# Performance work log

Measured on AMD Instinct MI355X. Metric: run time of the kernel, lower is better.

The kernel has to match this reference:

```python
import jax, jax.numpy as jnp
import numpy as np

EPS = 1e-7  # keras.backend.epsilon()
B, U, F = 1024, 256, 31
D = 1 + U + F  # features dim after concat


def setup_inputs() -> dict:
    key = jax.random.key(0)
    ks = jax.random.split(key, 9)
    s = 1.0 / np.sqrt(D)
    return {
        "last_cell": jax.random.uniform(ks[0], (B, U), dtype=jnp.float32),
        "input_precipitation": jax.random.uniform(ks[1], (B,), dtype=jnp.float32),
        "input_other_features": jax.random.normal(ks[2], (B, F), dtype=jnp.float32),
        "W_i": jax.random.normal(ks[3], (D, U), dtype=jnp.float32) * s,
        "b_i": jnp.zeros((U,), dtype=jnp.float32),
        "W_r": jax.random.normal(ks[4], (D, U * U), dtype=jnp.float32) * s,
        "b_r": jnp.zeros((U * U,), dtype=jnp.float32),
        "W_o": jax.random.normal(ks[5], (D, U), dtype=jnp.float32) * s,
        "b_o": jnp.zeros((U,), dtype=jnp.float32),
    }


def reference(last_cell, input_precipitation, input_other_features,
              W_i, b_i, W_r, b_r, W_o, b_o):
    # L1-normalize last cell state (mass fractions)
    l1 = jnp.sum(jnp.abs(last_cell), axis=-1, keepdims=True) + EPS
    last_cell_hat = last_cell / l1
    p = input_precipitation[:, None]  # [B,1]
    features = jnp.concatenate([p, last_cell_hat, input_other_features], axis=-1)  # [B,D]

    # input gate: sigmoid then L1-normalized across units (mass-conserving split)
    ig = jax.nn.sigmoid(features @ W_i + b_i)
    ig = ig / jnp.sum(jnp.abs(ig), axis=-1, keepdims=True)

    # redistribution matrix: relu, reshape [B,U,U], L1-normalize each row
    R = jax.nn.relu(features @ W_r + b_r).reshape(-1, U, U)
    R = R / jnp.sum(jnp.abs(R), axis=-1, keepdims=True)

    # output gate: sigmoid
    og = jax.nn.sigmoid(features @ W_o + b_o)

    cell_in = ig * p                                   # [B,U]
    cell_sys = jnp.einsum('bu,buv->bv', last_cell, R)  # batched (1xU)@(UxU)
    candidate = cell_in + cell_sys
    output = og * candidate
    cell = (1.0 - og) * candidate
    return (cell, output)
```

## Files before the change

### kernel.cpp

```cpp
#include <hip/hip_runtime.h>


#define EPS_L1 1e-7f

constexpr int BB  = 1024;
constexpr int U   = 256;
constexpr int F   = 31;
constexpr int D   = 1 + U + F;
constexpr int NBV = BB * U;
constexpr int NCH = D / 32;
constexpr int UIMGB = NCH * 16384;
constexpr size_t WTB_BYTES  = (size_t)258 * UIMGB;
constexpr size_t FEAT_BYTES = (size_t)BB * D * 2;

typedef float f32x4 __attribute__((ext_vector_type(4)));
typedef short bf16x8 __attribute__((ext_vector_type(8)));

__device__ __forceinline__ unsigned f2bf(float x) {
  union { float f; unsigned u; } v; v.f = x;
  unsigned r = v.u + 0x7FFFu + ((v.u >> 16) & 1u);
  return r >> 16;
}

__device__ __forceinline__ void barrier_lgkm() {
  asm volatile("s_waitcnt lgkmcnt(0)" ::: "memory");
  __builtin_amdgcn_sched_barrier(0);
  __builtin_amdgcn_s_barrier();
  __builtin_amdgcn_sched_barrier(0);
}

#define GLDS16(gp, lp)                                                        \
  __builtin_amdgcn_global_load_lds(                                          \
      (const __attribute__((address_space(1))) void*)(gp),                   \
      (__attribute__((address_space(3))) void*)(lp), 16, 0, 0)

#define MFMA16(a, b, c) __builtin_amdgcn_mfma_f32_16x16x32_bf16((a), (b), (c), 0, 0, 0)

__global__ __launch_bounds__(256) void k_prep(
    const float* __restrict__ lc, const float* __restrict__ p,
    const float* __restrict__ other,
    const float* __restrict__ Wi, const float* __restrict__ Wr,
    const float* __restrict__ Wo,
    short* __restrict__ WtB, short* __restrict__ featImg,
    float* __restrict__ cell_sys) {
  __shared__ unsigned tw[256][17];
  __shared__ float inv_s[64];
  const int bid = blockIdx.x, t = threadIdx.x;

  if (bid < 2322) {
    const int u = bid / 9, c = bid % 9;
    const float* src; long ld;
    if (u < 256)       { src = Wr + (size_t)u * 256; ld = 65536; }
    else if (u == 256) { src = Wi; ld = 256; }
    else               { src = Wo; ld = 256; }

    const int kp = t >> 4, f = t & 15;
    const float* r0 = src + (size_t)(c * 32 + 2 * kp) * ld;
    const float* r1 = r0 + ld;
#pragma unroll
    for (int i = 0; i < 4; ++i) {
      const int v0 = f * 4 + i * 64;
      const float4 a = *(const float4*)(r0 + v0);
      const float4 b = *(const float4*)(r1 + v0);
      tw[v0 + 0][kp] = f2bf(a.x) | (f2bf(b.x) << 16);
      tw[v0 + 1][kp] = f2bf(a.y) | (f2bf(b.y) << 16);
      tw[v0 + 2][kp] = f2bf(a.z) | (f2bf(b.z) << 16);
      tw[v0 + 3][kp] = f2bf(a.w) | (f2bf(b.w) << 16);
    }
    __syncthreads();

    const int lane = t & 63, wave = t >> 6;
    const int g = lane >> 4, l15 = lane & 15;
    short* dst = WtB + (size_t)u * 73728 + (size_t)c * 16 * 512;
#pragma unroll
    for (int ii = 0; ii < 4; ++ii) {
      const int n0 = wave * 4 + ii;
      const int row = n0 * 16 + l15;
      union { unsigned u4[4]; bf16x8 h; } cv;
#pragma unroll
      for (int j = 0; j < 4; ++j) cv.u4[j] = tw[row][g * 4 + j];
      *(bf16x8*)(dst + (size_t)n0 * 512 + lane * 8) = cv.h;
    }
  } else if (bid < 2338) {
    const int mb = bid - 2322;
    const int b0 = mb * 64;
    const int row = t >> 2, q = t & 3;
    const float4* lp = (const float4*)(lc + (size_t)(b0 + row) * 256 + q * 64);
    float s = 0.f;
#pragma unroll
    for (int j = 0; j < 16; ++j) {
      const float4 v = lp[j];
      s += fabsf(v.x) + fabsf(v.y) + fabsf(v.z) + fabsf(v.w);
    }
    s += __shfl_xor(s, 1, 64);
    s += __shfl_xor(s, 2, 64);
    if (q == 0) inv_s[row] = 1.f / (s + EPS_L1);
    __syncthreads();
#pragma unroll
    for (int i = 0; i < 9; ++i) {
      const int idx = i * 256 + t;
      const int reg = idx >> 6, l = idx & 63;
      const int c = reg >> 2, mt = reg & 3;
      const int lrow = mt * 16 + (l & 15);
      const int grow = b0 + lrow;
      const int k0 = c * 32 + (l >> 4) * 8;
      bf16x8 h;
#pragma unroll
      for (int j = 0; j < 8; ++j) {
        const int k = k0 + j;
        float v;
        if (k == 0) v = p[grow];
        else if (k <= 256) v = lc[(size_t)grow * 256 + (k - 1)] * inv_s[lrow];
        else v = other[(size_t)grow * 31 + (k - 257)];
        h[j] = (short)f2bf(v);
      }
      *(bf16x8*)(featImg + (size_t)mb * 18432 + (size_t)reg * 512 + l * 8) = h;
    }
  } else {
    float4* cs4 = (float4*)cell_sys;
    const int base = (bid - 2338) * 8192 + t;
    const float4 z = {0.f, 0.f, 0.f, 0.f};
#pragma unroll
    for (int k2 = 0; k2 < 32; ++k2) cs4[base + k2 * 256] = z;
  }
}

__global__ __launch_bounds__(512, 4) void k_heavyR10(
    const short* __restrict__ featImg, const short* __restrict__ WtB,
    const float* __restrict__ lc, const float* __restrict__ br,
    float* __restrict__ cell_sys) {
  __shared__ short aT[18432];
  __shared__ float rsum[2][64][4];
  __shared__ float lcs[8][64];

  const int t = threadIdx.x, lane = t & 63, wave = t >> 6;
  const int cq = wave & 3, rh = wave >> 2;
  const int quad = lane >> 4, l15 = lane & 15;
  const int bid = blockIdx.x;
  const int Mb = bid >> 5, ug = bid & 31;
  const int b0 = Mb * 64, u0 = ug * 8;

  {
    const char* gA = (const char*)featImg + (size_t)Mb * 36864;
    char* lA = (char*)aT;
#pragma unroll
    for (int i = 0; i < 5; ++i) {
      const int off = i * 8192 + t * 16;
      if (off < 36864) GLDS16(gA + off, lA + off);
    }
  }

  if (t < 64) {
    const float* lp = lc + (size_t)(b0 + t) * 256 + u0;
    const float4 v0 = *(const float4*)(lp);
    const float4 v1 = *(const float4*)(lp + 4);
    lcs[0][t] = v0.x; lcs[1][t] = v0.y; lcs[2][t] = v0.z; lcs[3][t] = v0.w;
    lcs[4][t] = v1.x; lcs[5][t] = v1.y; lcs[6][t] = v1.z; lcs[7][t] = v1.w;
  }

  const char* aB = (const char*)aT + rh * 2048 + lane * 16;
  const char* bB = (const char*)WtB + (size_t)u0 * UIMGB + cq * 4096 + lane * 16;

  f32x4 acc[2][4], outa[2][4];
#pragma unroll
  for (int m = 0; m < 2; ++m)
#pragma unroll
    for (int n = 0; n < 4; ++n)
#pragma unroll
      for (int r = 0; r < 4; ++r) { acc[m][n][r] = 0.f; outa[m][n][r] = 0.f; }

  bf16x8 bfr[3][4];
#pragma unroll
  for (int n = 0; n < 4; ++n) bfr[0][n] = *(const bf16x8*)(bB + n * 1024);
#pragma unroll
  for (int n = 0; n < 4; ++n) bfr[1][n] = *(const bf16x8*)(bB + 16384 + n * 1024);

  __syncthreads();

  for (int uu = 0; uu < 8; ++uu) {
    const int u = u0 + uu;
    float bv[4];

#pragma unroll
    for (int c = 0; c < 9; ++c) {
      if (c == 0) {
#pragma unroll
        for (int n = 0; n < 4; ++n)
          bv[n] = br[(size_t)u * 256 + cq * 64 + n * 16 + l15];
      }
#pragma unroll
      for (int n = 0; n < 4; ++n)
        bfr[(c + 2) % 3][n] = *(const bf16x8*)(bB + (c + 2) * 16384 + n * 1024);
      const bf16x8 a0 = *(const bf16x8*)(aB + c * 4096);
      const bf16x8 a1 = *(const bf16x8*)(aB + c * 4096 + 1024);
#pragma unroll
      for (int n = 0; n < 4; ++n) {
        acc[0][n] = MFMA16(a0, bfr[c % 3][n], acc[0][n]);
        acc[1][n] = MFMA16(a1, bfr[c % 3][n], acc[1][n]);
      }
    }
    bB += UIMGB;

    const int ub = uu & 1;
    float sm[2][4];
#pragma unroll
    for (int m = 0; m < 2; ++m)
#pragma unroll
      for (int r = 0; r < 4; ++r) {
        float sv = 0.f;
#pragma unroll
        for (int n = 0; n < 4; ++n) {
          const float rv = fmaxf(acc[m][n][r] + bv[n], 0.f);
          acc[m][n][r] = rv;
          sv += rv;
        }
        sm[m][r] = sv;
      }
#pragma unroll
    for (int msk = 1; msk < 16; msk <<= 1)
#pragma unroll
      for (int m = 0; m < 2; ++m)
#pragma unroll
        for (int r = 0; r < 4; ++r)
          sm[m][r] += __shfl_xor(sm[m][r], msk, 64);
    if (l15 == 0) {
#pragma unroll
      for (int m = 0; m < 2; ++m)
#pragma unroll
        for (int r = 0; r < 4; ++r)
          rsum[ub][rh * 32 + m * 16 + quad * 4 + r][cq] = sm[m][r];
    }
    barrier_lgkm();
#pragma unroll
    for (int m = 0; m < 2; ++m)
#pragma unroll
      for (int r = 0; r < 4; ++r) {
        const int row = rh * 32 + m * 16 + quad * 4 + r;
        const float4 rv = *(const float4*)&rsum[ub][row][0];
        const float tot = (rv.x + rv.y) + (rv.z + rv.w);
        const float alpha = lcs[uu][row] * __builtin_amdgcn_rcpf(tot);
#pragma unroll
        for (int n = 0; n < 4; ++n) {
          outa[m][n][r] = fmaf(alpha, acc[m][n][r], outa[m][n][r]);
          acc[m][n][r] = 0.f;
        }
      }
  }

#pragma unroll
  for (int m = 0; m < 2; ++m)
#pragma unroll
    for (int r = 0; r < 4; ++r) {
      const int grow = b0 + rh * 32 + m * 16 + quad * 4 + r;
#pragma unroll
      for (int n = 0; n < 4; ++n)
        atomicAdd(&cell_sys[(size_t)grow * 256 + cq * 64 + n * 16 + l15],
                  outa[m][n][r]);
    }
}

__global__ __launch_bounds__(512, 2) void k_postR8(
    const short* __restrict__ featImg, const short* __restrict__ WtB,
    const float* __restrict__ bi, const float* __restrict__ bo,
    const float* __restrict__ p, const float* __restrict__ cell_sys,
    float* __restrict__ dout) {
  __shared__ short aT9[9 * 512];
  __shared__ float cs[16 * 256];
  __shared__ float rsum[16][12];
  __shared__ float ps[16];

  const int t = threadIdx.x, lane = t & 63, cg = t >> 6;
  const int quad = lane >> 4, l15 = lane & 15;
  const int mb16 = blockIdx.x, b0 = mb16 * 16;
  const int mb = mb16 >> 2, mt = mb16 & 3;

  {
    const char* gsrc = (const char*)featImg + (size_t)mb * 36864 + mt * 1024;
    char* ldst = (char*)aT9;
    GLDS16(gsrc + (size_t)(t >> 6) * 4096 + (t & 63) * 16, ldst + t * 16);
    if (t < 64)
      GLDS16(gsrc + (size_t)8 * 4096 + t * 16, ldst + 8192 + t * 16);
  }
  if (t < 16) ps[t] = p[b0 + t];

  {
    const f32x4* pp = (const f32x4*)(cell_sys + (size_t)b0 * 256);
    ((f32x4*)cs)[t] = pp[t];
    ((f32x4*)cs)[512 + t] = pp[512 + t];
  }

  f32x4 acc[2];
#pragma unroll
  for (int n = 0; n < 2; ++n)
#pragma unroll
    for (int r = 0; r < 4; ++r) acc[n][r] = 0.f;

  const char* bptr = (const char*)WtB + (size_t)256 * UIMGB + cg * 2048 + lane * 16;
  bf16x8 cb0 = *(const bf16x8*)(bptr);
  bf16x8 cb1 = *(const bf16x8*)(bptr + 1024);
  bf16x8 nb0 = *(const bf16x8*)(bptr + 16384);
  bf16x8 nb1 = *(const bf16x8*)(bptr + 16384 + 1024);
  bptr += 32768;

  __syncthreads();

  float ig0[4], ig1[4], og0[4], og1[4];

#pragma unroll
  for (int g = 0; g < 2; ++g) {
    const float* bias = (g == 0) ? bi : bo;
    const float bv0 = bias[cg * 32 + l15];
    const float bv1 = bias[cg * 32 + 16 + l15];
#pragma unroll
    for (int c = 0; c < 9; ++c) {
      const bf16x8 pb0 = *(const bf16x8*)(bptr);
      const bf16x8 pb1 = *(const bf16x8*)(bptr + 1024);
      bptr += 16384;
      const bf16x8 a0 = *(const bf16x8*)((const char*)aT9 + c * 1024 + lane * 16);
      acc[0] = MFMA16(a0, cb0, acc[0]);
      acc[1] = MFMA16(a0, cb1, acc[1]);
      cb0 = nb0; cb1 = nb1; nb0 = pb0; nb1 = pb1;
    }

#pragma unroll
    for (int r = 0; r < 4; ++r) {
      const float v0 = 1.f / (1.f + __expf(-(acc[0][r] + bv0)));
      const float v1 = 1.f / (1.f + __expf(-(acc[1][r] + bv1)));
      if (g == 0) { ig0[r] = v0; ig1[r] = v1; }
      else        { og0[r] = v0; og1[r] = v1; }
      acc[0][r] = 0.f;
      acc[1][r] = 0.f;
    }

    if (g == 0) {
      float sm[4];
#pragma unroll
      for (int r = 0; r < 4; ++r) sm[r] = ig0[r] + ig1[r];
#pragma unroll
      for (int msk = 1; msk < 16; msk <<= 1)
#pragma unroll
        for (int r = 0; r < 4; ++r)
          sm[r] += __shfl_xor(sm[r], msk, 64);
      if (l15 == 0) {
#pragma unroll
        for (int r = 0; r < 4; ++r)
          rsum[quad * 4 + r][cg] = sm[r];
      }
      __syncthreads();
#pragma unroll
      for (int r = 0; r < 4; ++r) {
        const int row = quad * 4 + r;
        const float4 ra = *(const float4*)&rsum[row][0];
        const float4 rb = *(const float4*)&rsum[row][4];
        const float inv = 1.f / (((ra.x + ra.y) + (ra.z + ra.w)) +
                                 ((rb.x + rb.y) + (rb.z + rb.w)));
        ig0[r] *= inv;
        ig1[r] *= inv;
      }
    }
  }

#pragma unroll
  for (int r = 0; r < 4; ++r) {
    const int row = quad * 4 + r;
    const float pr = ps[row];
    const int ci = row * 256 + cg * 32 + l15;
    const size_t base = (size_t)(b0 + row) * 256 + cg * 32 + l15;
    {
      const float cand = fmaf(ig0[r], pr, cs[ci]);
      dout[base] = (1.f - og0[r]) * cand;
      dout[NBV + base] = og0[r] * cand;
    }
    {
      const float cand = fmaf(ig1[r], pr, cs[ci + 16]);
      dout[base + 16] = (1.f - og1[r]) * cand;
      dout[NBV + base + 16] = og1[r] * cand;
    }
  }
}

extern "C" void kernel_launch(void* const* d_in, const int* in_sizes, int n_in,
                              void* d_out, int out_size, void* d_ws, size_t ws_size,
                              hipStream_t stream) {
  const float* lc    = (const float*)d_in[0];
  const float* p     = (const float*)d_in[1];
  const float* other = (const float*)d_in[2];
  const float* Wi    = (const float*)d_in[3];
  const float* bi    = (const float*)d_in[4];
  const float* Wr    = (const float*)d_in[5];
  const float* br    = (const float*)d_in[6];
  const float* Wo    = (const float*)d_in[7];
  const float* bo    = (const float*)d_in[8];
  float* out = (float*)d_out;

  char* wsb = (char*)d_ws;
  short* WtB      = (short*)wsb;
  short* featImg  = (short*)(wsb + WTB_BYTES);
  float* cell_sys = (float*)(wsb + WTB_BYTES + FEAT_BYTES);

  k_prep<<<2346, 256, 0, stream>>>(lc, p, other, Wi, Wr, Wo, WtB, featImg, cell_sys);
  k_heavyR10<<<512, 512, 0, stream>>>(featImg, WtB, lc, br, cell_sys);
  k_postR8<<<64, 512, 0, stream>>>(featImg, WtB, bi, bo, p, cell_sys, out);
}
```

Before: 212.0 us.

## Retile heavy R kernel to 32x256 tiles with private partial buffers

The heavy redistribution kernel changes from 64-row by 8-unit tiles (512 blocks) to 32-row by 32-unit tiles (256 blocks). Each wave now covers all 256 output columns in 32-wide slices, so a block computes full R rows and takes the row L1 sums across 8 waves. When the workspace is large enough, each unit-group writes its own partial cell_sys slice instead of using atomics, and the post kernel sums the 8 partials. This is meant to cut atomic traffic and the A-tile LDS footprint, at the cost of fewer blocks (less parallelism), more partial-buffer traffic, and a k_prep that still zeroes only the first slice.

```diff
diff --git a/kernel.cpp b/kernel.cpp
--- a/kernel.cpp
+++ b/kernel.cpp
@@ -12,6 +12,8 @@
 constexpr int UIMGB = NCH * 16384;
 constexpr size_t WTB_BYTES  = (size_t)258 * UIMGB;
 constexpr size_t FEAT_BYTES = (size_t)BB * D * 2;
+constexpr size_t PART_BYTES = (size_t)8 * BB * U * 4;
+constexpr size_t NEED_PRIV  = WTB_BYTES + FEAT_BYTES + PART_BYTES;
 
 typedef float f32x4 __attribute__((ext_vector_type(4)));
 typedef short bf16x8 __attribute__((ext_vector_type(8)));
@@ -42,7 +44,7 @@
     const float* __restrict__ Wi, const float* __restrict__ Wr,
     const float* __restrict__ Wo,
     short* __restrict__ WtB, short* __restrict__ featImg,
-    float* __restrict__ cell_sys) {
+    float* __restrict__ partial) {
   __shared__ unsigned tw[256][17];
   __shared__ float inv_s[64];
   const int bid = blockIdx.x, t = threadIdx.x;
@@ -117,7 +119,7 @@
       *(bf16x8*)(featImg + (size_t)mb * 18432 + (size_t)reg * 512 + l * 8) = h;
     }
   } else {
-    float4* cs4 = (float4*)cell_sys;
+    float4* cs4 = (float4*)partial;
     const int base = (bid - 2338) * 8192 + t;
     const float4 z = {0.f, 0.f, 0.f, 0.f};
 #pragma unroll
@@ -125,81 +127,90 @@
   }
 }
 
-__global__ __launch_bounds__(512, 4) void k_heavyR10(
+template <bool PRIV>
+__global__ __launch_bounds__(512, 4) void k_heavyR12(
     const short* __restrict__ featImg, const short* __restrict__ WtB,
     const float* __restrict__ lc, const float* __restrict__ br,
-    float* __restrict__ cell_sys) {
-  __shared__ short aT[18432];
-  __shared__ float rsum[2][64][4];
-  __shared__ float lcs[8][64];
+    float* __restrict__ partial) {
+  __shared__ short aT[9216];
+  __shared__ float rsum[2][32][8];
+  __shared__ float lcs[32][33];
 
   const int t = threadIdx.x, lane = t & 63, wave = t >> 6;
-  const int cq = wave & 3, rh = wave >> 2;
+  const int cq = wave;
   const int quad = lane >> 4, l15 = lane & 15;
   const int bid = blockIdx.x;
-  const int Mb = bid >> 5, ug = bid & 31;
-  const int b0 = Mb * 64, u0 = ug * 8;
+  const int Mb = bid >> 3, ug = bid & 7;
+  const int b0 = Mb * 32, u0 = ug * 32;
+  const int mb = Mb >> 1, h2 = Mb & 1;
 
   {
-    const char* gA = (const char*)featImg + (size_t)Mb * 36864;
+    const char* gA = (const char*)featImg + (size_t)mb * 36864;
     char* lA = (char*)aT;
-#pragma unroll
-    for (int i = 0; i < 5; ++i) {
-      const int off = i * 8192 + t * 16;
-      if (off < 36864) GLDS16(gA + off, lA + off);
-    }
-  }
-
-  if (t < 64) {
-    const float* lp = lc + (size_t)(b0 + t) * 256 + u0;
-    const float4 v0 = *(const float4*)(lp);
-    const float4 v1 = *(const float4*)(lp + 4);
-    lcs[0][t] = v0.x; lcs[1][t] = v0.y; lcs[2][t] = v0.z; lcs[3][t] = v0.w;
-    lcs[4][t] = v1.x; lcs[5][t] = v1.y; lcs[6][t] = v1.z; lcs[7][t] = v1.w;
-  }
-
-  const char* aB = (const char*)aT + rh * 2048 + lane * 16;
-  const char* bB = (const char*)WtB + (size_t)u0 * UIMGB + cq * 4096 + lane * 16;
-
-  f32x4 acc[2][4], outa[2][4];
+    const int ch0 = wave;
+    GLDS16(gA + (size_t)((ch0 >> 1) * 4 + h2 * 2 + (ch0 & 1)) * 1024 + lane * 16,
+           lA + ch0 * 1024 + lane * 16);
+    const int ch1 = wave + 8;
+    GLDS16(gA + (size_t)((ch1 >> 1) * 4 + h2 * 2 + (ch1 & 1)) * 1024 + lane * 16,
+           lA + ch1 * 1024 + lane * 16);
+    if (wave < 2) {
+      const int ch2 = wave + 16;
+      GLDS16(gA + (size_t)((ch2 >> 1) * 4 + h2 * 2 + (ch2 & 1)) * 1024 + lane * 16,
+             lA + ch2 * 1024 + lane * 16);
+    }
+  }
+
+  if (t < 256) {
+    const int row = t >> 3, j4 = (t & 7) * 4;
+    const float4 v = *(const float4*)(lc + (size_t)(b0 + row) * 256 + u0 + j4);
+    lcs[j4 + 0][row] = v.x;
+    lcs[j4 + 1][row] = v.y;
+    lcs[j4 + 2][row] = v.z;
+    lcs[j4 + 3][row] = v.w;
+  }
+
+  const char* bW = (const char*)WtB + (size_t)u0 * UIMGB + cq * 2048 + lane * 16;
+
+  f32x4 acc[2][2], outa[2][2];
 #pragma unroll
   for (int m = 0; m < 2; ++m)
 #pragma unroll
-    for (int n = 0; n < 4; ++n)
+    for (int n = 0; n < 2; ++n)
 #pragma unroll
       for (int r = 0; r < 4; ++r) { acc[m][n][r] = 0.f; outa[m][n][r] = 0.f; }
 
-  bf16x8 bfr[3][4];
-#pragma unroll
-  for (int n = 0; n < 4; ++n) bfr[0][n] = *(const bf16x8*)(bB + n * 1024);
-#pragma unroll
-  for (int n = 0; n < 4; ++n) bfr[1][n] = *(const bf16x8*)(bB + 16384 + n * 1024);
+  bf16x8 bfr[3][2];
+#pragma unroll
+  for (int n = 0; n < 2; ++n) bfr[0][n] = *(const bf16x8*)(bW + n * 1024);
+#pragma unroll
+  for (int n = 0; n < 2; ++n) bfr[1][n] = *(const bf16x8*)(bW + 16384 + n * 1024);
 
   __syncthreads();
 
-  for (int uu = 0; uu < 8; ++uu) {
+  for (int uu = 0; uu < 32; ++uu) {
     const int u = u0 + uu;
-    float bv[4];
+    float bv[2];
 
 #pragma unroll
     for (int c = 0; c < 9; ++c) {
+      const int cc = uu * 9 + c;
       if (c == 0) {
 #pragma unroll
-        for (int n = 0; n < 4; ++n)
-          bv[n] = br[(size_t)u * 256 + cq * 64 + n * 16 + l15];
-      }
-#pragma unroll
-      for (int n = 0; n < 4; ++n)
-        bfr[(c + 2) % 3][n] = *(const bf16x8*)(bB + (c + 2) * 16384 + n * 1024);
-      const bf16x8 a0 = *(const bf16x8*)(aB + c * 4096);
-      const bf16x8 a1 = *(const bf16x8*)(aB + c * 4096 + 1024);
-#pragma unroll
-      for (int n = 0; n < 4; ++n) {
-        acc[0][n] = MFMA16(a0, bfr[c % 3][n], acc[0][n]);
-        acc[1][n] = MFMA16(a1, bfr[c % 3][n], acc[1][n]);
-      }
-    }
-    bB += UIMGB;
+        for (int n = 0; n < 2; ++n)
+          bv[n] = br[(size_t)u * 256 + cq * 32 + n * 16 + l15];
+      }
+#pragma unroll
+      for (int n = 0; n < 2; ++n)
+        bfr[(cc + 2) % 3][n] =
+            *(const bf16x8*)(bW + (size_t)(cc + 2) * 16384 + n * 1024);
+      const bf16x8 a0 = *(const bf16x8*)((const char*)aT + (c * 2 + 0) * 1024 + lane * 16);
+      const bf16x8 a1 = *(const bf16x8*)((const char*)aT + (c * 2 + 1) * 1024 + lane * 16);
+      const int s = cc % 3;
+      acc[0][0] = MFMA16(a0, bfr[s][0], acc[0][0]);
+      acc[0][1] = MFMA16(a0, bfr[s][1], acc[0][1]);
+      acc[1][0] = MFMA16(a1, bfr[s][0], acc[1][0]);
+      acc[1][1] = MFMA16(a1, bfr[s][1], acc[1][1]);
+    }
 
     const int ub = uu & 1;
     float sm[2][4];
@@ -209,7 +220,7 @@
       for (int r = 0; r < 4; ++r) {
         float sv = 0.f;
 #pragma unroll
-        for (int n = 0; n < 4; ++n) {
+        for (int n = 0; n < 2; ++n) {
           const float rv = fmaxf(acc[m][n][r] + bv[n], 0.f);
           acc[m][n][r] = rv;
           sv += rv;
@@ -228,41 +239,48 @@
       for (int m = 0; m < 2; ++m)
 #pragma unroll
         for (int r = 0; r < 4; ++r)
-          rsum[ub][rh * 32 + m * 16 + quad * 4 + r][cq] = sm[m][r];
+          rsum[ub][m * 16 + quad * 4 + r][cq] = sm[m][r];
     }
     barrier_lgkm();
 #pragma unroll
     for (int m = 0; m < 2; ++m)
 #pragma unroll
       for (int r = 0; r < 4; ++r) {
-        const int row = rh * 32 + m * 16 + quad * 4 + r;
-        const float4 rv = *(const float4*)&rsum[ub][row][0];
-        const float tot = (rv.x + rv.y) + (rv.z + rv.w);
+        const int row = m * 16 + quad * 4 + r;
+        const float4 ra = *(const float4*)&rsum[ub][row][0];
+        const float4 rb = *(const float4*)&rsum[ub][row][4];
+        const float tot = ((ra.x + ra.y) + (ra.z + ra.w)) +
+                          ((rb.x + rb.y) + (rb.z + rb.w));
         const float alpha = lcs[uu][row] * __builtin_amdgcn_rcpf(tot);
 #pragma unroll
-        for (int n = 0; n < 4; ++n) {
+        for (int n = 0; n < 2; ++n) {
           outa[m][n][r] = fmaf(alpha, acc[m][n][r], outa[m][n][r]);
           acc[m][n][r] = 0.f;
         }
       }
   }
 
+  const size_t pb = PRIV ? ((size_t)ug << 18) : 0;
 #pragma unroll
   for (int m = 0; m < 2; ++m)
 #pragma unroll
     for (int r = 0; r < 4; ++r) {
-      const int grow = b0 + rh * 32 + m * 16 + quad * 4 + r;
-#pragma unroll
-      for (int n = 0; n < 4; ++n)
-        atomicAdd(&cell_sys[(size_t)grow * 256 + cq * 64 + n * 16 + l15],
-                  outa[m][n][r]);
-    }
-}
-
-__global__ __launch_bounds__(512, 2) void k_postR8(
+      const int grow = b0 + m * 16 + quad * 4 + r;
+      const size_t base = pb + (size_t)grow * 256 + cq * 32 + l15;
+      if (PRIV) {
+        partial[base]      = outa[m][0][r];
+        partial[base + 16] = outa[m][1][r];
+      } else {
+        atomicAdd(&partial[base],      outa[m][0][r]);
+        atomicAdd(&partial[base + 16], outa[m][1][r]);
+      }
+    }
+}
+
+__global__ __launch_bounds__(512, 2) void k_postR12(
     const short* __restrict__ featImg, const short* __restrict__ WtB,
     const float* __restrict__ bi, const float* __restrict__ bo,
-    const float* __restrict__ p, const float* __restrict__ cell_sys,
+    const float* __restrict__ p, const float* __restrict__ partial, int npart,
     float* __restrict__ dout) {
   __shared__ short aT9[9 * 512];
   __shared__ float cs[16 * 256];
@@ -284,9 +302,15 @@
   if (t < 16) ps[t] = p[b0 + t];
 
   {
-    const f32x4* pp = (const f32x4*)(cell_sys + (size_t)b0 * 256);
-    ((f32x4*)cs)[t] = pp[t];
-    ((f32x4*)cs)[512 + t] = pp[512 + t];
+    const float* pbase = partial + (size_t)b0 * 256;
+    f32x4 s0 = {0.f, 0.f, 0.f, 0.f}, s1 = {0.f, 0.f, 0.f, 0.f};
+    for (int ug = 0; ug < npart; ++ug) {
+      const f32x4* pp = (const f32x4*)(pbase + (size_t)ug * 262144);
+      s0 += pp[t];
+      s1 += pp[512 + t];
+    }
+    ((f32x4*)cs)[t] = s0;
+    ((f32x4*)cs)[512 + t] = s1;
   }
 
   f32x4 acc[2];
@@ -396,9 +420,14 @@
   char* wsb = (char*)d_ws;
   short* WtB      = (short*)wsb;
   short* featImg  = (short*)(wsb + WTB_BYTES);
-  float* cell_sys = (float*)(wsb + WTB_BYTES + FEAT_BYTES);
-
-  k_prep<<<2346, 256, 0, stream>>>(lc, p, other, Wi, Wr, Wo, WtB, featImg, cell_sys);
-  k_heavyR10<<<512, 512, 0, stream>>>(featImg, WtB, lc, br, cell_sys);
-  k_postR8<<<64, 512, 0, stream>>>(featImg, WtB, bi, bo, p, cell_sys, out);
-}
+  float* partial  = (float*)(wsb + WTB_BYTES + FEAT_BYTES);
+  const bool priv = (ws_size >= NEED_PRIV);
+
+  k_prep<<<2346, 256, 0, stream>>>(lc, p, other, Wi, Wr, Wo, WtB, featImg, partial);
+  if (priv)
+    k_heavyR12<true><<<256, 512, 0, stream>>>(featImg, WtB, lc, br, partial);
+  else
+    k_heavyR12<false><<<256, 512, 0, stream>>>(featImg, WtB, lc, br, partial);
+  k_postR12<<<64, 512, 0, stream>>>(featImg, WtB, bi, bo, p, partial,
+                                    priv ? 8 : 1, out);
+}
```

Result: slower. 226.8 us (+7.0%).

## Restructure heavy R kernel so each wave owns full U rows, removing block barriers

Applied to the files above, without the earlier changes.

The heavy kernel now gives each wave all 256 output columns of an R row (16 MFMA tiles), so the row L1 sum is finished with intra-wave shuffles instead of a cross-wave LDS exchange and block barrier per u. Blocks now cover 16 u values each over 256 blocks, bias rows are staged into LDS, and results go into 8 partial buffers that the post kernel sums. This removes the per-iteration barrier and atomic contention in exchange for larger register use (32 accumulators), lower occupancy, B fragments loaded without the prefetch pipeline, and extra partial-buffer zeroing and traffic.

```diff
diff --git a/kernel.cpp b/kernel.cpp
--- a/kernel.cpp
+++ b/kernel.cpp
@@ -22,13 +22,6 @@
   return r >> 16;
 }
 
-__device__ __forceinline__ void barrier_lgkm() {
-  asm volatile("s_waitcnt lgkmcnt(0)" ::: "memory");
-  __builtin_amdgcn_sched_barrier(0);
-  __builtin_amdgcn_s_barrier();
-  __builtin_amdgcn_sched_barrier(0);
-}
-
 #define GLDS16(gp, lp)                                                        \
   __builtin_amdgcn_global_load_lds(                                          \
       (const __attribute__((address_space(1))) void*)(gp),                   \
@@ -42,7 +35,7 @@
     const float* __restrict__ Wi, const float* __restrict__ Wr,
     const float* __restrict__ Wo,
     short* __restrict__ WtB, short* __restrict__ featImg,
-    float* __restrict__ cell_sys) {
+    float* __restrict__ partial) {
   __shared__ unsigned tw[256][17];
   __shared__ float inv_s[64];
   const int bid = blockIdx.x, t = threadIdx.x;
@@ -117,7 +110,7 @@
       *(bf16x8*)(featImg + (size_t)mb * 18432 + (size_t)reg * 512 + l * 8) = h;
     }
   } else {
-    float4* cs4 = (float4*)cell_sys;
+    float4* cs4 = (float4*)partial;
     const int base = (bid - 2338) * 8192 + t;
     const float4 z = {0.f, 0.f, 0.f, 0.f};
 #pragma unroll
@@ -125,20 +118,23 @@
   }
 }
 
-__global__ __launch_bounds__(512, 4) void k_heavyR10(
+__global__ __launch_bounds__(512, 2) void k_heavyR13(
     const short* __restrict__ featImg, const short* __restrict__ WtB,
     const float* __restrict__ lc, const float* __restrict__ br,
-    float* __restrict__ cell_sys) {
+    float* __restrict__ partial) {
   __shared__ short aT[18432];
-  __shared__ float rsum[2][64][4];
-  __shared__ float lcs[8][64];
-
-  const int t = threadIdx.x, lane = t & 63, wave = t >> 6;
-  const int cq = wave & 3, rh = wave >> 2;
-  const int quad = lane >> 4, l15 = lane & 15;
+  __shared__ float brs[16 * 256];
+  __shared__ float lcs[16][66];
+
+  const int t = threadIdx.x, lane = t & 63, w = t >> 6;
+  const int l15 = lane & 15, quad = lane >> 4;
   const int bid = blockIdx.x;
-  const int Mb = bid >> 5, ug = bid & 31;
-  const int b0 = Mb * 64, u0 = ug * 8;
+  const int Mb = bid >> 4, q = bid & 15;
+  const int ug = q & 7, uh = q >> 3;
+  const int b0 = Mb * 64;
+  const int u0 = ug * 32 + uh * 16;
+  const int s = w & 3, uhh = w >> 2;
+  const int uw0 = u0 + uhh * 8;
 
   {
     const char* gA = (const char*)featImg + (size_t)Mb * 36864;
@@ -148,121 +144,88 @@
       const int off = i * 8192 + t * 16;
       if (off < 36864) GLDS16(gA + off, lA + off);
     }
-  }
-
-  if (t < 64) {
-    const float* lp = lc + (size_t)(b0 + t) * 256 + u0;
-    const float4 v0 = *(const float4*)(lp);
-    const float4 v1 = *(const float4*)(lp + 4);
-    lcs[0][t] = v0.x; lcs[1][t] = v0.y; lcs[2][t] = v0.z; lcs[3][t] = v0.w;
-    lcs[4][t] = v1.x; lcs[5][t] = v1.y; lcs[6][t] = v1.z; lcs[7][t] = v1.w;
-  }
-
-  const char* aB = (const char*)aT + rh * 2048 + lane * 16;
-  const char* bB = (const char*)WtB + (size_t)u0 * UIMGB + cq * 4096 + lane * 16;
-
-  f32x4 acc[2][4], outa[2][4];
-#pragma unroll
-  for (int m = 0; m < 2; ++m)
-#pragma unroll
-    for (int n = 0; n < 4; ++n)
-#pragma unroll
-      for (int r = 0; r < 4; ++r) { acc[m][n][r] = 0.f; outa[m][n][r] = 0.f; }
-
-  bf16x8 bfr[3][4];
-#pragma unroll
-  for (int n = 0; n < 4; ++n) bfr[0][n] = *(const bf16x8*)(bB + n * 1024);
-#pragma unroll
-  for (int n = 0; n < 4; ++n) bfr[1][n] = *(const bf16x8*)(bB + 16384 + n * 1024);
+    const char* gB = (const char*)(br + (size_t)u0 * 256);
+    char* lB = (char*)brs;
+    GLDS16(gB + t * 16, lB + t * 16);
+    GLDS16(gB + 8192 + t * 16, lB + 8192 + t * 16);
+  }
+#pragma unroll
+  for (int i = 0; i < 2; ++i) {
+    const int idx = i * 512 + t;
+    const int row = idx >> 4, j = idx & 15;
+    lcs[j][row] = lc[(size_t)(b0 + row) * 256 + u0 + j];
+  }
+
+  f32x4 acc[16], outa[16];
+#pragma unroll
+  for (int n = 0; n < 16; ++n)
+#pragma unroll
+    for (int r = 0; r < 4; ++r) { acc[n][r] = 0.f; outa[n][r] = 0.f; }
 
   __syncthreads();
 
+  const char* aBase = (const char*)aT + s * 1024 + lane * 16;
+  const char* bBase = (const char*)WtB + (size_t)uw0 * UIMGB + lane * 16;
+
   for (int uu = 0; uu < 8; ++uu) {
-    const int u = u0 + uu;
-    float bv[4];
+    const char* bU = bBase + (size_t)uu * UIMGB;
 
 #pragma unroll
     for (int c = 0; c < 9; ++c) {
-      if (c == 0) {
-#pragma unroll
-        for (int n = 0; n < 4; ++n)
-          bv[n] = br[(size_t)u * 256 + cq * 64 + n * 16 + l15];
-      }
-#pragma unroll
-      for (int n = 0; n < 4; ++n)
-        bfr[(c + 2) % 3][n] = *(const bf16x8*)(bB + (c + 2) * 16384 + n * 1024);
-      const bf16x8 a0 = *(const bf16x8*)(aB + c * 4096);
-      const bf16x8 a1 = *(const bf16x8*)(aB + c * 4096 + 1024);
-#pragma unroll
-      for (int n = 0; n < 4; ++n) {
-        acc[0][n] = MFMA16(a0, bfr[c % 3][n], acc[0][n]);
-        acc[1][n] = MFMA16(a1, bfr[c % 3][n], acc[1][n]);
-      }
-    }
-    bB += UIMGB;
-
-    const int ub = uu & 1;
-    float sm[2][4];
-#pragma unroll
-    for (int m = 0; m < 2; ++m)
+      const bf16x8 a = *(const bf16x8*)(aBase + c * 4096);
+      const char* bC = bU + (size_t)c * 16384;
+#pragma unroll
+      for (int n = 0; n < 16; ++n) {
+        const bf16x8 b = *(const bf16x8*)(bC + n * 1024);
+        acc[n] = MFMA16(a, b, acc[n]);
+      }
+    }
+
+    const int ul = uhh * 8 + uu;
+    float sm[4];
+#pragma unroll
+    for (int r = 0; r < 4; ++r) sm[r] = 0.f;
+#pragma unroll
+    for (int n = 0; n < 16; ++n) {
+      const float bv = brs[ul * 256 + n * 16 + l15];
 #pragma unroll
       for (int r = 0; r < 4; ++r) {
-        float sv = 0.f;
-#pragma unroll
-        for (int n = 0; n < 4; ++n) {
-          const float rv = fmaxf(acc[m][n][r] + bv[n], 0.f);
-          acc[m][n][r] = rv;
-          sv += rv;
-        }
-        sm[m][r] = sv;
-      }
+        const float rv = fmaxf(acc[n][r] + bv, 0.f);
+        acc[n][r] = rv;
+        sm[r] += rv;
+      }
+    }
 #pragma unroll
     for (int msk = 1; msk < 16; msk <<= 1)
 #pragma unroll
-      for (int m = 0; m < 2; ++m)
-#pragma unroll
-        for (int r = 0; r < 4; ++r)
-          sm[m][r] += __shfl_xor(sm[m][r], msk, 64);
-    if (l15 == 0) {
-#pragma unroll
-      for (int m = 0; m < 2; ++m)
-#pragma unroll
-        for (int r = 0; r < 4; ++r)
-          rsum[ub][rh * 32 + m * 16 + quad * 4 + r][cq] = sm[m][r];
-    }
-    barrier_lgkm();
-#pragma unroll
-    for (int m = 0; m < 2; ++m)
-#pragma unroll
-      for (int r = 0; r < 4; ++r) {
-        const int row = rh * 32 + m * 16 + quad * 4 + r;
-        const float4 rv = *(const float4*)&rsum[ub][row][0];
-        const float tot = (rv.x + rv.y) + (rv.z + rv.w);
-        const float alpha = lcs[uu][row] * __builtin_amdgcn_rcpf(tot);
-#pragma unroll
-        for (int n = 0; n < 4; ++n) {
-          outa[m][n][r] = fmaf(alpha, acc[m][n][r], outa[m][n][r]);
-          acc[m][n][r] = 0.f;
-        }
-      }
-  }
-
-#pragma unroll
-  for (int m = 0; m < 2; ++m)
+      for (int r = 0; r < 4; ++r)
+        sm[r] += __shfl_xor(sm[r], msk, 64);
 #pragma unroll
     for (int r = 0; r < 4; ++r) {
-      const int grow = b0 + rh * 32 + m * 16 + quad * 4 + r;
-#pragma unroll
-      for (int n = 0; n < 4; ++n)
-        atomicAdd(&cell_sys[(size_t)grow * 256 + cq * 64 + n * 16 + l15],
-                  outa[m][n][r]);
-    }
-}
-
-__global__ __launch_bounds__(512, 2) void k_postR8(
+      const int row = s * 16 + quad * 4 + r;
+      const float alpha = lcs[ul][row] * __builtin_amdgcn_rcpf(sm[r]);
+#pragma unroll
+      for (int n = 0; n < 16; ++n) {
+        outa[n][r] = fmaf(alpha, acc[n][r], outa[n][r]);
+        acc[n][r] = 0.f;
+      }
+    }
+  }
+
+  float* pc = partial + ((size_t)ug << 18);
+#pragma unroll
+  for (int r = 0; r < 4; ++r) {
+    const int grow = b0 + s * 16 + quad * 4 + r;
+#pragma unroll
+    for (int n = 0; n < 16; ++n)
+      atomicAdd(&pc[(size_t)grow * 256 + n * 16 + l15], outa[n][r]);
+  }
+}
+
+__global__ __launch_bounds__(512, 2) void k_postR12(
     const short* __restrict__ featImg, const short* __restrict__ WtB,
     const float* __restrict__ bi, const float* __restrict__ bo,
-    const float* __restrict__ p, const float* __restrict__ cell_sys,
+    const float* __restrict__ p, const float* __restrict__ partial, int npart,
     float* __restrict__ dout) {
   __shared__ short aT9[9 * 512];
   __shared__ float cs[16 * 256];
@@ -284,9 +247,15 @@
   if (t < 16) ps[t] = p[b0 + t];
 
   {
-    const f32x4* pp = (const f32x4*)(cell_sys + (size_t)b0 * 256);
-    ((f32x4*)cs)[t] = pp[t];
-    ((f32x4*)cs)[512 + t] = pp[512 + t];
+    const float* pbase = partial + (size_t)b0 * 256;
+    f32x4 s0 = {0.f, 0.f, 0.f, 0.f}, s1 = {0.f, 0.f, 0.f, 0.f};
+    for (int ug = 0; ug < npart; ++ug) {
+      const f32x4* pp = (const f32x4*)(pbase + (size_t)ug * 262144);
+      s0 += pp[t];
+      s1 += pp[512 + t];
+    }
+    ((f32x4*)cs)[t] = s0;
+    ((f32x4*)cs)[512 + t] = s1;
   }
 
   f32x4 acc[2];
@@ -396,9 +365,9 @@
   char* wsb = (char*)d_ws;
   short* WtB      = (short*)wsb;
   short* featImg  = (short*)(wsb + WTB_BYTES);
-  float* cell_sys = (float*)(wsb + WTB_BYTES + FEAT_BYTES);
-
-  k_prep<<<2346, 256, 0, stream>>>(lc, p, other, Wi, Wr, Wo, WtB, featImg, cell_sys);
-  k_heavyR10<<<512, 512, 0, stream>>>(featImg, WtB, lc, br, cell_sys);
-  k_postR8<<<64, 512, 0, stream>>>(featImg, WtB, bi, bo, p, cell_sys, out);
-}
+  float* partial  = (float*)(wsb + WTB_BYTES + FEAT_BYTES);
+
+  k_prep<<<2402, 256, 0, stream>>>(lc, p, other, Wi, Wr, Wo, WtB, featImg, partial);
+  k_heavyR13<<<256, 512, 0, stream>>>(featImg, WtB, lc, br, partial);
+  k_postR12<<<64, 512, 0, stream>>>(featImg, WtB, bi, bo, p, partial, 8, out);
+}
```

Result: slower. 294.7 us (+39.0%).
